# Kernel optimization log

Measured on AMD Instinct MI355X. Metric: run time of the kernel, lower is better.

The kernel has to match this reference:

```python
import jax, jax.numpy as jnp
import numpy as np


def setup_inputs() -> dict:
    key = jax.random.key(0)
    k1, k2, k3 = jax.random.split(key, 3)
    S, B, H, D = 1024, 32, 512, 1024  # max_len, batch, bin_rnn_size, bin_rep_size
    hidden = jax.random.normal(k1, (2, B, H), dtype=jnp.float32)
    encoder_outputs = jax.random.normal(k2, (S, B, D), dtype=jnp.float32)
    # nn.Linear(D, D) params; scale W for numerically sane softmax logits
    W = jax.random.normal(k3, (D, D), dtype=jnp.float32) / np.float32(np.sqrt(D))
    b = jnp.zeros((D,), dtype=jnp.float32)
    return {"hidden": hidden, "encoder_outputs": encoder_outputs, "W": W, "b": b}


def reference(hidden, encoder_outputs, W, b):
    # method == 'general'
    B = hidden.shape[1]
    # torch.reshape((-1, B, 2H)).squeeze() == C-order flatten -> [B, 2H]
    h = hidden.reshape(B, -1)                                   # [B, D]
    energy = jnp.einsum('sbd,ed->sbe', encoder_outputs, W) + b  # Linear: x @ W.T + b
    # batch_product_luong + sum over features == contraction
    attn_energies = jnp.einsum('bd,sbd->bs', h, energy)         # [B, S]
    alpha = jax.nn.softmax(attn_energies, axis=1)[:, None, :]   # [B, 1, S]
    # alpha.bmm(encoder_outputs.transpose(0,1)) -> [B, 1, D]
    reps = jnp.einsum('bos,sbd->bod', alpha, encoder_outputs)
    return (reps, alpha)
```

## Files before the change

### kernel.cpp

```cpp
#include <hip/hip_runtime.h>

#define S 1024
#define B 32
#define D 1024
#define NCH 32
#define CH (S / NCH)
#define RPW (CH / 4)
#define NPAIR (RPW / 2)
#define ECH 8
#define EC 128

#define PG_OFF   0
#define LOG_OFF  (PG_OFF + ECH * B * D)
#define MARR_OFF (LOG_OFF + B * S)
#define LARR_OFF (MARR_OFF + NCH * B)
#define PACC_OFF (LARR_OFF + NCH * B)

__global__ __launch_bounds__(256) void kG2(const float* __restrict__ hid,
                                           const float* __restrict__ W,
                                           float* __restrict__ ws) {
    const int tid = threadIdx.x;
    const int dc  = blockIdx.x;
    const int ec  = blockIdx.y;
    __shared__ float h_sh[EC * 33];
    #pragma unroll
    for (int k = 0; k < (EC * B) / 256; ++k) {
        int lin = tid + k * 256;
        int e = lin >> 5;
        int b = lin & 31;
        h_sh[e * 33 + b] = hid[b * D + ec * EC + e];
    }
    __syncthreads();

    const int b  = tid >> 3;
    const int dq = tid & 7;
    const float4* W4 = (const float4*)W;
    float4 a4 = {0.f, 0.f, 0.f, 0.f};
    #pragma unroll 8
    for (int e = 0; e < EC; ++e) {
        float  h = h_sh[e * 33 + b];
        float4 w = W4[(size_t)(ec * EC + e) * (D / 4) + dc * 8 + dq];
        a4.x = fmaf(h, w.x, a4.x);
        a4.y = fmaf(h, w.y, a4.y);
        a4.z = fmaf(h, w.z, a4.z);
        a4.w = fmaf(h, w.w, a4.w);
    }
    ((float4*)(ws + PG_OFF + ((size_t)ec * B + b) * D + dc * 32))[dq] = a4;
}

__global__ __launch_bounds__(256) void kB(const float* __restrict__ enc,
                                          float* __restrict__ ws) {
    const int tid  = threadIdx.x;
    const int lane = tid & 63;
    const int wid  = tid >> 6;
    const int c    = blockIdx.x;
    const int b    = blockIdx.y;

    float* pg     = ws + PG_OFF;
    float* logits = ws + LOG_OFF;
    float* marr   = ws + MARR_OFF;
    float* larr   = ws + LARR_OFF;
    float* pacc   = ws + PACC_OFF;

    __shared__ float4 g_sh[256];
    __shared__ float4 sacc[4 * 256];
    __shared__ float sm[4], sl[4];

    const float4* encb = (const float4*)enc;
    const int row0 = c * CH + wid * RPW;
    const size_t rstride = (size_t)B * (D / 4);
    size_t base = ((size_t)row0 * B + b) * (D / 4) + lane;

    float4 cur[8], nxt[8];
    #pragma unroll
    for (int j = 0; j < 4; ++j) {
        cur[j]     = encb[base + j * 64];
        cur[4 + j] = encb[base + rstride + j * 64];
    }
    #pragma unroll
    for (int j = 0; j < 4; ++j) {
        nxt[j]     = encb[base + 2 * rstride + j * 64];
        nxt[4 + j] = encb[base + 3 * rstride + j * 64];
    }

    {
        float4 s4 = {0.f, 0.f, 0.f, 0.f};
        #pragma unroll
        for (int ec = 0; ec < ECH; ++ec) {
            float4 v = ((const float4*)(pg + (size_t)(ec * B + b) * D))[tid];
            s4.x += v.x; s4.y += v.y; s4.z += v.z; s4.w += v.w;
        }
        g_sh[tid] = s4;
    }
    __syncthreads();
    float4 gv[4];
    #pragma unroll
    for (int j = 0; j < 4; ++j) gv[j] = g_sh[j * 64 + lane];

    float m = -3.0e38f, l = 0.f;
    float4 acc[4] = {{0,0,0,0},{0,0,0,0},{0,0,0,0},{0,0,0,0}};

    #pragma unroll
    for (int p = 0; p < NPAIR; ++p) {
        float pd0 = 0.f, pd1 = 0.f;
        #pragma unroll
        for (int j = 0; j < 4; ++j) {
            pd0 += cur[j].x * gv[j].x + cur[j].y * gv[j].y +
                   cur[j].z * gv[j].z + cur[j].w * gv[j].w;
            pd1 += cur[4+j].x * gv[j].x + cur[4+j].y * gv[j].y +
                   cur[4+j].z * gv[j].z + cur[4+j].w * gv[j].w;
        }
        #pragma unroll
        for (int off = 1; off < 64; off <<= 1) {
            pd0 += __shfl_xor(pd0, off, 64);
            pd1 += __shfl_xor(pd1, off, 64);
        }
        if (lane == 0) {
            logits[b * S + row0 + 2 * p]     = pd0;
            logits[b * S + row0 + 2 * p + 1] = pd1;
        }
        float mn  = fmaxf(m, pd0);
        float sc0 = __expf(m - mn);
        float pA  = __expf(pd0 - mn);
        float mn2 = fmaxf(mn, pd1);
        float sc1 = __expf(mn - mn2);
        float pB  = __expf(pd1 - mn2);
        float s01 = sc0 * sc1;
        float a0  = pA * sc1;
        l = l * s01 + a0 + pB;
        #pragma unroll
        for (int j = 0; j < 4; ++j) {
            acc[j].x = acc[j].x * s01 + a0 * cur[j].x + pB * cur[4+j].x;
            acc[j].y = acc[j].y * s01 + a0 * cur[j].y + pB * cur[4+j].y;
            acc[j].z = acc[j].z * s01 + a0 * cur[j].z + pB * cur[4+j].z;
            acc[j].w = acc[j].w * s01 + a0 * cur[j].w + pB * cur[4+j].w;
        }
        m = mn2;
        if (p + 1 < NPAIR) {
            #pragma unroll
            for (int j = 0; j < 8; ++j) cur[j] = nxt[j];
        }
        if (p + 2 < NPAIR) {
            size_t nb = base + (size_t)(2 * (p + 2)) * rstride;
            #pragma unroll
            for (int j = 0; j < 4; ++j) {
                nxt[j]     = encb[nb + j * 64];
                nxt[4 + j] = encb[nb + rstride + j * 64];
            }
        }
    }

    #pragma unroll
    for (int j = 0; j < 4; ++j) sacc[wid * 256 + j * 64 + lane] = acc[j];
    if (lane == 0) { sm[wid] = m; sl[wid] = l; }
    __syncthreads();
    float mg = fmaxf(fmaxf(sm[0], sm[1]), fmaxf(sm[2], sm[3]));
    float4 r = {0.f, 0.f, 0.f, 0.f};
    float lsum = 0.f;
    #pragma unroll
    for (int w = 0; w < 4; ++w) {
        float fw = __expf(sm[w] - mg);
        float4 a = sacc[w * 256 + wid * 64 + lane];
        r.x += a.x * fw; r.y += a.y * fw; r.z += a.z * fw; r.w += a.w * fw;
        lsum += sl[w] * fw;
    }
    ((float4*)pacc)[(size_t)(c * B + b) * (D / 4) + tid] = r;
    if (tid == 0) { marr[c * B + b] = mg; larr[c * B + b] = lsum; }
}

__global__ __launch_bounds__(256) void kC(float* __restrict__ out,
                                          const float* __restrict__ ws) {
    const int tid = threadIdx.x;
    const int q   = blockIdx.x;
    const int b   = blockIdx.y;
    const float* logits = ws + LOG_OFF;
    const float* marr   = ws + MARR_OFF;
    const float* larr   = ws + LARR_OFF;
    const float* pacc   = ws + PACC_OFF;

    __shared__ float shm[NCH], shl[NCH], shf[NCH];
    if (tid < NCH) { shm[tid] = marr[tid * B + b]; shl[tid] = larr[tid * B + b]; }
    __syncthreads();
    float mg = -3.0e38f;
    #pragma unroll
    for (int cc = 0; cc < NCH; ++cc) mg = fmaxf(mg, shm[cc]);
    if (tid < NCH) shf[tid] = __expf(shm[tid] - mg);
    __syncthreads();
    float lg = 0.f;
    #pragma unroll
    for (int cc = 0; cc < NCH; ++cc) lg += shl[cc] * shf[cc];
    const float inv = 1.f / lg;

    if (tid < 64) {
        const int d4 = q * 64 + tid;
        float4 racc = {0.f, 0.f, 0.f, 0.f};
        #pragma unroll 4
        for (int cc = 0; cc < NCH; ++cc) {
            float  fc = shf[cc];
            float4 v  = ((const float4*)pacc)[(size_t)(cc * B + b) * (D / 4) + d4];
            racc.x += v.x * fc; racc.y += v.y * fc;
            racc.z += v.z * fc; racc.w += v.w * fc;
        }
        float4 rep = {racc.x * inv, racc.y * inv, racc.z * inv, racc.w * inv};
        ((float4*)out)[b * (D / 4) + d4] = rep;
    }
    const int s = q * 256 + tid;
    out[B * D + b * S + s] = __expf(logits[b * S + s] - mg) * inv;
}

extern "C" void kernel_launch(void* const* d_in, const int* in_sizes, int n_in,
                              void* d_out, int out_size, void* d_ws, size_t ws_size,
                              hipStream_t stream) {
    const float* hid = (const float*)d_in[0];
    const float* enc = (const float*)d_in[1];
    const float* W   = (const float*)d_in[2];

    float* out = (float*)d_out;
    float* ws  = (float*)d_ws;

    kG2<<<dim3(32, ECH), 256, 0, stream>>>(hid, W, ws);
    kB<<<dim3(NCH, B), 256, 0, stream>>>(enc, ws);
    kC<<<dim3(4, B), 256, 0, stream>>>(out, ws);
}
```

Baseline: 42.96 us.

## Split sequence into 64 chunks with all four rows loaded upfront per wave

Doubles the number of sequence chunks so each wave handles only four rows, loaded all at once instead of through a pipelined online-softmax loop. This doubles the grid of the main kernel, giving more memory-level parallelism and simpler math per wave, at the cost of twice as many partial accumulators for the final combine kernel to read. It also changes the index mapping in the hidden-load loop of the first kernel to coalesce global reads of the hidden vector.

```diff
diff --git a/kernel.cpp b/kernel.cpp
--- a/kernel.cpp
+++ b/kernel.cpp
@@ -3,10 +3,9 @@
 #define S 1024
 #define B 32
 #define D 1024
-#define NCH 32
+#define NCH 64
 #define CH (S / NCH)
-#define RPW (CH / 4)
-#define NPAIR (RPW / 2)
+#define RPW 4
 #define ECH 8
 #define EC 128
 
@@ -26,8 +25,8 @@
     #pragma unroll
     for (int k = 0; k < (EC * B) / 256; ++k) {
         int lin = tid + k * 256;
-        int e = lin >> 5;
-        int b = lin & 31;
+        int e = lin & (EC - 1);
+        int b = lin >> 7;
         h_sh[e * 33 + b] = hid[b * D + ec * EC + e];
     }
     __syncthreads();
@@ -71,17 +70,12 @@
     const size_t rstride = (size_t)B * (D / 4);
     size_t base = ((size_t)row0 * B + b) * (D / 4) + lane;
 
-    float4 cur[8], nxt[8];
-    #pragma unroll
-    for (int j = 0; j < 4; ++j) {
-        cur[j]     = encb[base + j * 64];
-        cur[4 + j] = encb[base + rstride + j * 64];
-    }
-    #pragma unroll
-    for (int j = 0; j < 4; ++j) {
-        nxt[j]     = encb[base + 2 * rstride + j * 64];
-        nxt[4 + j] = encb[base + 3 * rstride + j * 64];
-    }
+    float4 ev[16];
+    #pragma unroll
+    for (int r = 0; r < 4; ++r)
+        #pragma unroll
+        for (int j = 0; j < 4; ++j)
+            ev[r * 4 + j] = encb[base + (size_t)r * rstride + j * 64];
 
     {
         float4 s4 = {0.f, 0.f, 0.f, 0.f};
@@ -97,57 +91,39 @@
     #pragma unroll
     for (int j = 0; j < 4; ++j) gv[j] = g_sh[j * 64 + lane];
 
-    float m = -3.0e38f, l = 0.f;
-    float4 acc[4] = {{0,0,0,0},{0,0,0,0},{0,0,0,0},{0,0,0,0}};
-
-    #pragma unroll
-    for (int p = 0; p < NPAIR; ++p) {
-        float pd0 = 0.f, pd1 = 0.f;
-        #pragma unroll
-        for (int j = 0; j < 4; ++j) {
-            pd0 += cur[j].x * gv[j].x + cur[j].y * gv[j].y +
-                   cur[j].z * gv[j].z + cur[j].w * gv[j].w;
-            pd1 += cur[4+j].x * gv[j].x + cur[4+j].y * gv[j].y +
-                   cur[4+j].z * gv[j].z + cur[4+j].w * gv[j].w;
-        }
-        #pragma unroll
-        for (int off = 1; off < 64; off <<= 1) {
-            pd0 += __shfl_xor(pd0, off, 64);
-            pd1 += __shfl_xor(pd1, off, 64);
-        }
-        if (lane == 0) {
-            logits[b * S + row0 + 2 * p]     = pd0;
-            logits[b * S + row0 + 2 * p + 1] = pd1;
-        }
-        float mn  = fmaxf(m, pd0);
-        float sc0 = __expf(m - mn);
-        float pA  = __expf(pd0 - mn);
-        float mn2 = fmaxf(mn, pd1);
-        float sc1 = __expf(mn - mn2);
-        float pB  = __expf(pd1 - mn2);
-        float s01 = sc0 * sc1;
-        float a0  = pA * sc1;
-        l = l * s01 + a0 + pB;
-        #pragma unroll
-        for (int j = 0; j < 4; ++j) {
-            acc[j].x = acc[j].x * s01 + a0 * cur[j].x + pB * cur[4+j].x;
-            acc[j].y = acc[j].y * s01 + a0 * cur[j].y + pB * cur[4+j].y;
-            acc[j].z = acc[j].z * s01 + a0 * cur[j].z + pB * cur[4+j].z;
-            acc[j].w = acc[j].w * s01 + a0 * cur[j].w + pB * cur[4+j].w;
-        }
-        m = mn2;
-        if (p + 1 < NPAIR) {
-            #pragma unroll
-            for (int j = 0; j < 8; ++j) cur[j] = nxt[j];
-        }
-        if (p + 2 < NPAIR) {
-            size_t nb = base + (size_t)(2 * (p + 2)) * rstride;
-            #pragma unroll
-            for (int j = 0; j < 4; ++j) {
-                nxt[j]     = encb[nb + j * 64];
-                nxt[4 + j] = encb[nb + rstride + j * 64];
-            }
-        }
+    float d0 = 0.f, d1 = 0.f, d2 = 0.f, d3 = 0.f;
+    #pragma unroll
+    for (int j = 0; j < 4; ++j) {
+        d0 += ev[0+j].x*gv[j].x + ev[0+j].y*gv[j].y + ev[0+j].z*gv[j].z + ev[0+j].w*gv[j].w;
+        d1 += ev[4+j].x*gv[j].x + ev[4+j].y*gv[j].y + ev[4+j].z*gv[j].z + ev[4+j].w*gv[j].w;
+        d2 += ev[8+j].x*gv[j].x + ev[8+j].y*gv[j].y + ev[8+j].z*gv[j].z + ev[8+j].w*gv[j].w;
+        d3 += ev[12+j].x*gv[j].x + ev[12+j].y*gv[j].y + ev[12+j].z*gv[j].z + ev[12+j].w*gv[j].w;
+    }
+    #pragma unroll
+    for (int off = 1; off < 64; off <<= 1) {
+        d0 += __shfl_xor(d0, off, 64);
+        d1 += __shfl_xor(d1, off, 64);
+        d2 += __shfl_xor(d2, off, 64);
+        d3 += __shfl_xor(d3, off, 64);
+    }
+    if (lane == 0) {
+        logits[b * S + row0 + 0] = d0;
+        logits[b * S + row0 + 1] = d1;
+        logits[b * S + row0 + 2] = d2;
+        logits[b * S + row0 + 3] = d3;
+    }
+
+    float m = fmaxf(fmaxf(d0, d1), fmaxf(d2, d3));
+    float p0 = __expf(d0 - m), p1 = __expf(d1 - m),
+          p2 = __expf(d2 - m), p3 = __expf(d3 - m);
+    float l = (p0 + p1) + (p2 + p3);
+    float4 acc[4];
+    #pragma unroll
+    for (int j = 0; j < 4; ++j) {
+        acc[j].x = p0*ev[0+j].x + p1*ev[4+j].x + p2*ev[8+j].x + p3*ev[12+j].x;
+        acc[j].y = p0*ev[0+j].y + p1*ev[4+j].y + p2*ev[8+j].y + p3*ev[12+j].y;
+        acc[j].z = p0*ev[0+j].z + p1*ev[4+j].z + p2*ev[8+j].z + p3*ev[12+j].z;
+        acc[j].w = p0*ev[0+j].w + p1*ev[4+j].w + p2*ev[8+j].w + p3*ev[12+j].w;
     }
 
     #pragma unroll
```

Result: slower. 44.56 us (+3.7%).
